# Optimization experiments

Measured on AMD Instinct MI355X. Metric: run time of the kernel, lower is better.

The kernel has to match this reference:

```python
import jax, jax.numpy as jnp
import numpy as np

B, N, E, D = 8, 4096, 65536, 256


def setup_inputs() -> dict:
    key = jax.random.key(0)
    ks = jax.random.split(key, 4)
    return {
        "node_features": jax.random.normal(ks[0], (B, N, D), dtype=jnp.float32),
        "W": jax.random.normal(ks[1], (D, D), dtype=jnp.float32) * (1.0 / np.sqrt(D)),
        "b": jnp.zeros((D,), dtype=jnp.float32),
        "gamma": jnp.ones((D,), dtype=jnp.float32),
        "beta": jnp.zeros((D,), dtype=jnp.float32),
        "edge_index": jax.random.randint(ks[2], (B, 2, E), 0, N, dtype=jnp.int64),
        "node_mask": jax.random.randint(ks[3], (B, N), 0, 2, dtype=jnp.int32),
    }


def reference(node_features, W, b, gamma, beta, edge_index, node_mask):
    # Linear projection: h = x @ W^T + b   (nn.Linear convention, W: [out, in])
    h = jnp.einsum("bni,oi->bno", node_features, W) + b  # [B, N, D]
    batch, n_nodes, d = h.shape
    n_edges = edge_index.shape[2]

    src = edge_index[:, 0, :]  # [B, E]
    tgt = edge_index[:, 1, :]  # [B, E]

    nm = node_mask.astype(h.dtype)  # [B, N]
    # edge valid iff both endpoints are valid nodes
    emask = jnp.take_along_axis(nm, src, axis=1) * jnp.take_along_axis(nm, tgt, axis=1)  # [B, E]

    # gather source features, mask invalid edges
    msg = jnp.take_along_axis(h, src[..., None], axis=1) * emask[..., None]  # [B, E, D]

    # batched scatter-add via flat segment_sum with per-batch offsets
    seg_ids = (tgt + jnp.arange(batch, dtype=tgt.dtype)[:, None] * n_nodes).reshape(-1)
    agg = jax.ops.segment_sum(msg.reshape(batch * n_edges, d), seg_ids,
                              num_segments=batch * n_nodes).reshape(batch, n_nodes, d)

    h = h + agg / jnp.sqrt(jnp.asarray(n_nodes, h.dtype))

    # dropout is identity in eval mode
    # LayerNorm over last dim (eps = 1e-5, torch default)
    mu = jnp.mean(h, axis=-1, keepdims=True)
    var = jnp.mean((h - mu) ** 2, axis=-1, keepdims=True)
    h = (h - mu) * jax.lax.rsqrt(var + 1e-5) * gamma + beta

    h = jax.nn.relu(h)
    return h * nm[..., None]
```

## Files before the change

kernel.cpp:

```cpp
#include <hip/hip_runtime.h>
#include <hip/hip_bf16.h>

#define NN 4096
#define DIM 256
#define NE 65536
#define TOT_NODES 32768
#define TOT_EDGES 524288

__device__ __forceinline__ float ldf(const void* p, int isbf, size_t i) {
    return isbf ? __bfloat162float(((const __hip_bfloat16*)p)[i]) : ((const float*)p)[i];
}
__device__ __forceinline__ void stf(void* p, int isbf, size_t i, float v) {
    if (isbf) ((__hip_bfloat16*)p)[i] = __float2bfloat16(v);
    else      ((float*)p)[i] = v;
}
__device__ __forceinline__ int ldi(const void* p, int is64, size_t i) {
    return is64 ? (int)((const long long*)p)[i] : ((const int*)p)[i];
}

__global__ void detect_kernel(const void* ei, const void* nm, const void* x, int* flags) {
    const int t = threadIdx.x;
    const long long ev = ((const long long*)ei)[t];
    const unsigned long long okE = __ballot(ev >= 0 && ev < NN);
    const long long mv = ((const long long*)nm)[t];
    const unsigned long long okM = __ballot(mv == 0 || mv == 1);
    const unsigned int w = ((const unsigned int*)x)[t];
    const int e = (w >> 7) & 0xFF;
    const unsigned long long okF = __ballot(e >= 100 && e <= 140);
    if (t == 0) {
        flags[0] = (okE == ~0ULL) ? 1 : 0;
        flags[1] = (okM == ~0ULL) ? 1 : 0;
        flags[2] = (__popcll(okF) >= 40) ? 1 : 0;
    }
}

__global__ __launch_bounds__(256)
void init_kernel(int* __restrict__ counts) {
    counts[blockIdx.x * 256 + threadIdx.x] = 0;
}


typedef __attribute__((ext_vector_type(8))) __bf16 bf16x8;
typedef __attribute__((ext_vector_type(4))) float  f32x4;

__device__ __forceinline__ unsigned short f2bf(float f) {
    unsigned u = __float_as_uint(f);
    u = (u + 0x7fffu + ((u >> 16) & 1u)) >> 16;
    return (unsigned short)u;
}
__device__ __forceinline__ float bf2f(unsigned short h) {
    return __uint_as_float(((unsigned)h) << 16);
}
__device__ __forceinline__ void cvt_hilo(float4 f, ushort4* hi, ushort4* lo) {
    const unsigned short h0 = f2bf(f.x), h1 = f2bf(f.y), h2 = f2bf(f.z), h3 = f2bf(f.w);
    *hi = make_ushort4(h0, h1, h2, h3);
    *lo = make_ushort4(f2bf(f.x - bf2f(h0)), f2bf(f.y - bf2f(h1)),
                       f2bf(f.z - bf2f(h2)), f2bf(f.w - bf2f(h3)));
}
__device__ __forceinline__ bf16x8 frag_ld(const unsigned short* base, int row, int col) {
    const int byte = ((row * 64 + col) * 2) ^ ((row & 7) << 4);
    return *(const bf16x8*)((const char*)base + byte);
}
__device__ __forceinline__ void gload16(const void* g, void* l) {
    __builtin_amdgcn_global_load_lds(
        (const __attribute__((address_space(1))) unsigned int*)g,
        (__attribute__((address_space(3))) unsigned int*)l, 16, 0, 0);
}

__global__ __launch_bounds__(512)
void gemm_kernel(const void* __restrict__ x, const void* __restrict__ w,
                 const void* __restrict__ bias, const int* __restrict__ flags,
                 float* __restrict__ h)
{
    __shared__ unsigned short Ahi[128 * 64];
    __shared__ unsigned short Bhi[256 * 64];
    __shared__ unsigned short Alo[128 * 64];
    __shared__ unsigned short Blo[256 * 64];

    const int fbf = flags[2];
    const int t = threadIdx.x;
    const int lane = t & 63;
    const int wid = t >> 6;
    const int wr = wid >> 2;
    const int wc = wid & 3;
    const int m0 = (int)blockIdx.x * 128;

    f32x4 acc[4][4];
#pragma unroll
    for (int mi = 0; mi < 4; ++mi)
#pragma unroll
        for (int nj = 0; nj < 4; ++nj)
            acc[mi][nj] = (f32x4){0.f, 0.f, 0.f, 0.f};

    for (int kt = 0; kt < 4; ++kt) {
        const int k0 = kt * 64;
        if (fbf) {
            const unsigned short* xp = (const unsigned short*)x;
            const unsigned short* wp = (const unsigned short*)w;
#pragma unroll
            for (int i = 0; i < 2; ++i) {
                const int s = i * 512 + t;
                const int row = s >> 3, cg = (s & 7) ^ (row & 7);
                gload16(xp + (size_t)(m0 + row) * 256 + k0 + cg * 8, &Ahi[s * 8]);
            }
#pragma unroll
            for (int i = 0; i < 4; ++i) {
                const int s = i * 512 + t;
                const int row = s >> 3, cg = (s & 7) ^ (row & 7);
                gload16(wp + (size_t)row * 256 + k0 + cg * 8, &Bhi[s * 8]);
            }
        } else {
            const float* xp = (const float*)x;
            const float* wp = (const float*)w;
#pragma unroll
            for (int i = 0; i < 2; ++i) {
                const int s = i * 512 + t;
                const int row = s >> 3, cg = (s & 7) ^ (row & 7);
                const float* src = xp + (size_t)(m0 + row) * 256 + k0 + cg * 8;
                const float4 f0 = *(const float4*)src, f1 = *(const float4*)(src + 4);
                ushort4 h0, l0, h1, l1;
                cvt_hilo(f0, &h0, &l0); cvt_hilo(f1, &h1, &l1);
                *(ushort4*)&Ahi[s * 8]     = h0; *(ushort4*)&Ahi[s * 8 + 4] = h1;
                *(ushort4*)&Alo[s * 8]     = l0; *(ushort4*)&Alo[s * 8 + 4] = l1;
            }
#pragma unroll
            for (int i = 0; i < 4; ++i) {
                const int s = i * 512 + t;
                const int row = s >> 3, cg = (s & 7) ^ (row & 7);
                const float* src = wp + (size_t)row * 256 + k0 + cg * 8;
                const float4 f0 = *(const float4*)src, f1 = *(const float4*)(src + 4);
                ushort4 h0, l0, h1, l1;
                cvt_hilo(f0, &h0, &l0); cvt_hilo(f1, &h1, &l1);
                *(ushort4*)&Bhi[s * 8]     = h0; *(ushort4*)&Bhi[s * 8 + 4] = h1;
                *(ushort4*)&Blo[s * 8]     = l0; *(ushort4*)&Blo[s * 8 + 4] = l1;
            }
        }
        __syncthreads();

#pragma unroll
        for (int kk = 0; kk < 64; kk += 32) {
            const int lr = lane & 15;
            const int lk = kk + ((lane >> 4) << 3);
            bf16x8 aH[4], bH[4];
#pragma unroll
            for (int mi = 0; mi < 4; ++mi)
                aH[mi] = frag_ld(Ahi, wr * 64 + mi * 16 + lr, lk);
#pragma unroll
            for (int nj = 0; nj < 4; ++nj)
                bH[nj] = frag_ld(Bhi, wc * 64 + nj * 16 + lr, lk);
#pragma unroll
            for (int mi = 0; mi < 4; ++mi)
#pragma unroll
                for (int nj = 0; nj < 4; ++nj)
                    acc[mi][nj] = __builtin_amdgcn_mfma_f32_16x16x32_bf16(
                        aH[mi], bH[nj], acc[mi][nj], 0, 0, 0);
            if (!fbf) {
                bf16x8 aL[4], bL[4];
#pragma unroll
                for (int mi = 0; mi < 4; ++mi)
                    aL[mi] = frag_ld(Alo, wr * 64 + mi * 16 + lr, lk);
#pragma unroll
                for (int nj = 0; nj < 4; ++nj)
                    bL[nj] = frag_ld(Blo, wc * 64 + nj * 16 + lr, lk);
#pragma unroll
                for (int mi = 0; mi < 4; ++mi)
#pragma unroll
                    for (int nj = 0; nj < 4; ++nj) {
                        acc[mi][nj] = __builtin_amdgcn_mfma_f32_16x16x32_bf16(
                            aH[mi], bL[nj], acc[mi][nj], 0, 0, 0);
                        acc[mi][nj] = __builtin_amdgcn_mfma_f32_16x16x32_bf16(
                            aL[mi], bH[nj], acc[mi][nj], 0, 0, 0);
                    }
            }
        }
        __syncthreads();
    }

    const int lr = lane & 15;
    const int r4 = (lane >> 4) << 2;
#pragma unroll
    for (int nj = 0; nj < 4; ++nj) {
        const int n = wc * 64 + nj * 16 + lr;
        const float bv = ldf(bias, fbf, n);
#pragma unroll
        for (int mi = 0; mi < 4; ++mi) {
            const int rb = m0 + wr * 64 + mi * 16 + r4;
#pragma unroll
            for (int r = 0; r < 4; ++r)
                h[(size_t)(rb + r) * 256 + n] = acc[mi][nj][r] + bv;
        }
    }
}

__global__ __launch_bounds__(256)
void count_kernel(const void* __restrict__ ei, const void* __restrict__ nm,
                  const int* __restrict__ flags, int* __restrict__ counts)
{
    const int e64 = flags[0], m64 = flags[1];
    const int tid = blockIdx.x * 256 + threadIdx.x;
    const int b = tid >> 16;
    const int e = tid & (NE - 1);
    const size_t eb = (size_t)b * 2 * NE;
    const int src = ldi(ei, e64, eb + e);
    const int tgt = ldi(ei, e64, eb + NE + e);
    const size_t mb = (size_t)b * NN;
    if (ldi(nm, m64, mb + src) && ldi(nm, m64, mb + tgt))
        atomicAdd(&counts[b * NN + tgt], 1);
}

__global__ __launch_bounds__(256)
void scan_kernel(int* __restrict__ counts, int* __restrict__ offsets)
{
    __shared__ int sums[256];
    const int t = threadIdx.x;
    const int base = t * 128;
    int s = 0;
    for (int i = 0; i < 128; ++i) s += counts[base + i];
    sums[t] = s;
    __syncthreads();
    for (int off = 1; off < 256; off <<= 1) {
        int v = (t >= off) ? sums[t - off] : 0;
        __syncthreads();
        sums[t] += v;
        __syncthreads();
    }
    int run = sums[t] - s;
    for (int i = 0; i < 128; ++i) {
        const int c = counts[base + i];
        offsets[base + i] = run;
        counts[base + i] = run;
        run += c;
    }
    if (t == 255) offsets[TOT_NODES] = sums[255];
}

__global__ __launch_bounds__(256)
void fill_kernel(const void* __restrict__ ei, const void* __restrict__ nm,
                 const int* __restrict__ flags,
                 int* __restrict__ cursor, int* __restrict__ bucket)
{
    const int e64 = flags[0], m64 = flags[1];
    const int tid = blockIdx.x * 256 + threadIdx.x;
    const int b = tid >> 16;
    const int e = tid & (NE - 1);
    const size_t eb = (size_t)b * 2 * NE;
    const int src = ldi(ei, e64, eb + e);
    const int tgt = ldi(ei, e64, eb + NE + e);
    const size_t mb = (size_t)b * NN;
    if (ldi(nm, m64, mb + src) && ldi(nm, m64, mb + tgt)) {
        int pos = atomicAdd(&cursor[b * NN + tgt], 1);
        bucket[pos] = src;
    }
}

__global__ __launch_bounds__(64)
void node_kernel(const float* __restrict__ h, const int* __restrict__ offsets,
                 const int* __restrict__ bucket, const void* __restrict__ nm,
                 const int* __restrict__ flags,
                 const void* __restrict__ gamma, const void* __restrict__ beta,
                 void* __restrict__ out)
{
    const int bt = blockIdx.x;
    const int lane = threadIdx.x;
    const int m64 = flags[1], fbf = flags[2];
    const size_t o4 = (size_t)bt * 64 + lane;
    if (!ldi(nm, m64, bt)) {
        if (fbf) ((ushort4*)out)[o4] = make_ushort4(0, 0, 0, 0);
        else     ((float4*)out)[o4]  = make_float4(0.f, 0.f, 0.f, 0.f);
        return;
    }
    const int b = bt >> 12;
    const float4* hb = (const float4*)h + ((size_t)b << 12) * 64;
    const float4 self = ((const float4*)h)[o4];
    const int s0 = offsets[bt], s1 = offsets[bt + 1];
    float4 a0 = make_float4(0.f, 0.f, 0.f, 0.f), a1 = a0, a2 = a0, a3 = a0;
    int j = s0;
    for (; j + 4 <= s1; j += 4) {
        const float4 v0 = hb[(size_t)bucket[j]     * 64 + lane];
        const float4 v1 = hb[(size_t)bucket[j + 1] * 64 + lane];
        const float4 v2 = hb[(size_t)bucket[j + 2] * 64 + lane];
        const float4 v3 = hb[(size_t)bucket[j + 3] * 64 + lane];
        a0.x += v0.x; a0.y += v0.y; a0.z += v0.z; a0.w += v0.w;
        a1.x += v1.x; a1.y += v1.y; a1.z += v1.z; a1.w += v1.w;
        a2.x += v2.x; a2.y += v2.y; a2.z += v2.z; a2.w += v2.w;
        a3.x += v3.x; a3.y += v3.y; a3.z += v3.z; a3.w += v3.w;
    }
    for (; j < s1; ++j) {
        const float4 v = hb[(size_t)bucket[j] * 64 + lane];
        a0.x += v.x; a0.y += v.y; a0.z += v.z; a0.w += v.w;
    }
    float4 acc;
    acc.x = self.x + ((a0.x + a1.x) + (a2.x + a3.x)) * 0.015625f;
    acc.y = self.y + ((a0.y + a1.y) + (a2.y + a3.y)) * 0.015625f;
    acc.z = self.z + ((a0.z + a1.z) + (a2.z + a3.z)) * 0.015625f;
    acc.w = self.w + ((a0.w + a1.w) + (a2.w + a3.w)) * 0.015625f;

    float v1r = (acc.x + acc.y) + (acc.z + acc.w);
    float v2r = (acc.x * acc.x + acc.y * acc.y) + (acc.z * acc.z + acc.w * acc.w);
#pragma unroll
    for (int off = 32; off > 0; off >>= 1) {
        v1r += __shfl_xor(v1r, off, 64);
        v2r += __shfl_xor(v2r, off, 64);
    }
    const float mu  = v1r * (1.f / 256.f);
    const float var = v2r * (1.f / 256.f) - mu * mu;
    const float inv = rsqrtf(var + 1e-5f);
    const int d0 = lane * 4;
    float y0 = (acc.x - mu) * inv * ldf(gamma, fbf, d0)     + ldf(beta, fbf, d0);
    float y1 = (acc.y - mu) * inv * ldf(gamma, fbf, d0 + 1) + ldf(beta, fbf, d0 + 1);
    float y2 = (acc.z - mu) * inv * ldf(gamma, fbf, d0 + 2) + ldf(beta, fbf, d0 + 2);
    float y3 = (acc.w - mu) * inv * ldf(gamma, fbf, d0 + 3) + ldf(beta, fbf, d0 + 3);
    y0 = fmaxf(y0, 0.f); y1 = fmaxf(y1, 0.f); y2 = fmaxf(y2, 0.f); y3 = fmaxf(y3, 0.f);
    if (fbf) ((ushort4*)out)[o4] = make_ushort4(f2bf(y0), f2bf(y1), f2bf(y2), f2bf(y3));
    else     ((float4*)out)[o4]  = make_float4(y0, y1, y2, y3);
}

static float g_sentinel[256];

extern "C" void kernel_launch(void* const* d_in, const int* in_sizes, int n_in,
                              void* d_out, int out_size, void* d_ws, size_t ws_size,
                              hipStream_t stream)
{
    (void)in_sizes; (void)n_in; (void)out_size;
    const void* x     = d_in[0];
    const void* W     = d_in[1];
    const void* bias  = d_in[2];
    const void* gamma = d_in[3];
    const void* beta  = d_in[4];
    const void* ei    = d_in[5];
    const void* nm    = d_in[6];

    char* ws = (char*)d_ws;
    int* flags   = (int*)ws;
    int* counts  = (int*)(ws + 256);
    int* offsets = (int*)(ws + 131328);
    int* bucket  = (int*)(ws + 262656);
    float* h     = (float*)(ws + 2359808);

    int fail = 0;
    hipGetLastError();
#define CHK(stage) do { if (!fail && hipGetLastError() != hipSuccess) fail = (stage); } while (0)

    detect_kernel<<<1, 64, 0, stream>>>(ei, nm, x, flags);                       CHK(1);
    init_kernel<<<TOT_NODES / 256, 256, 0, stream>>>(counts);                    CHK(2);
    gemm_kernel<<<TOT_NODES / 128, 512, 0, stream>>>(x, W, bias, flags, h);      CHK(3);
    count_kernel<<<TOT_EDGES / 256, 256, 0, stream>>>(ei, nm, flags, counts);    CHK(4);
    scan_kernel<<<1, 256, 0, stream>>>(counts, offsets);                         CHK(5);
    fill_kernel<<<TOT_EDGES / 256, 256, 0, stream>>>(ei, nm, flags, counts, bucket); CHK(6);
    node_kernel<<<TOT_NODES, 64, 0, stream>>>(h, offsets, bucket, nm, flags,
                                              gamma, beta, d_out);               CHK(7);
#undef CHK

    if (fail) {
        for (int i = 0; i < 256; ++i) g_sentinel[i] = 10000.f * (float)fail;
        hipMemcpyAsync(d_out, g_sentinel, sizeof(g_sentinel),
                       hipMemcpyHostToDevice, stream);
    }
}
```

Measured before the change: 172.2 us.

## Double-buffer GEMM loads, merge init/detect, vectorize edge kernels, batch node blocks

Merges the flag-detection and counter-zeroing kernels into one launch, which drops a launch. The bf16 GEMM path now double-buffers its LDS tiles so the next k-tile's async loads overlap the MFMA work, cutting the barriers per tile. The count and fill kernels each handle two edges per thread using vector index loads. The scan now reads counts coalesced, and node_kernel packs four nodes per 256-thread block, using the post-fill cursor array as segment ends instead of offsets[bt+1]. The fp32 path reuses the two LDS buffers as hi/lo planes, so its per-tile behaviour stays the same.

```diff
diff --git a/kernel.cpp b/kernel.cpp
--- a/kernel.cpp
+++ b/kernel.cpp
@@ -10,33 +10,30 @@
 __device__ __forceinline__ float ldf(const void* p, int isbf, size_t i) {
     return isbf ? __bfloat162float(((const __hip_bfloat16*)p)[i]) : ((const float*)p)[i];
 }
-__device__ __forceinline__ void stf(void* p, int isbf, size_t i, float v) {
-    if (isbf) ((__hip_bfloat16*)p)[i] = __float2bfloat16(v);
-    else      ((float*)p)[i] = v;
-}
 __device__ __forceinline__ int ldi(const void* p, int is64, size_t i) {
     return is64 ? (int)((const long long*)p)[i] : ((const int*)p)[i];
 }
 
-__global__ void detect_kernel(const void* ei, const void* nm, const void* x, int* flags) {
+__global__ __launch_bounds__(256)
+void init_detect_kernel(const void* ei, const void* nm, const void* x,
+                        int* __restrict__ flags, int* __restrict__ counts)
+{
     const int t = threadIdx.x;
-    const long long ev = ((const long long*)ei)[t];
-    const unsigned long long okE = __ballot(ev >= 0 && ev < NN);
-    const long long mv = ((const long long*)nm)[t];
-    const unsigned long long okM = __ballot(mv == 0 || mv == 1);
-    const unsigned int w = ((const unsigned int*)x)[t];
-    const int e = (w >> 7) & 0xFF;
-    const unsigned long long okF = __ballot(e >= 100 && e <= 140);
-    if (t == 0) {
-        flags[0] = (okE == ~0ULL) ? 1 : 0;
-        flags[1] = (okM == ~0ULL) ? 1 : 0;
-        flags[2] = (__popcll(okF) >= 40) ? 1 : 0;
-    }
-}
-
-__global__ __launch_bounds__(256)
-void init_kernel(int* __restrict__ counts) {
-    counts[blockIdx.x * 256 + threadIdx.x] = 0;
+    counts[blockIdx.x * 256 + t] = 0;
+    if (blockIdx.x == 0 && t < 64) {
+        const long long ev = ((const long long*)ei)[t];
+        const unsigned long long okE = __ballot(ev >= 0 && ev < NN);
+        const long long mv = ((const long long*)nm)[t];
+        const unsigned long long okM = __ballot(mv == 0 || mv == 1);
+        const unsigned int w = ((const unsigned int*)x)[t];
+        const int e = (w >> 7) & 0xFF;
+        const unsigned long long okF = __ballot(e >= 100 && e <= 140);
+        if (t == 0) {
+            flags[0] = (okE == ~0ULL) ? 1 : 0;
+            flags[1] = (okM == ~0ULL) ? 1 : 0;
+            flags[2] = (__popcll(okF) >= 40) ? 1 : 0;
+        }
+    }
 }
 
 
@@ -72,10 +69,8 @@
                  const void* __restrict__ bias, const int* __restrict__ flags,
                  float* __restrict__ h)
 {
-    __shared__ unsigned short Ahi[128 * 64];
-    __shared__ unsigned short Bhi[256 * 64];
-    __shared__ unsigned short Alo[128 * 64];
-    __shared__ unsigned short Blo[256 * 64];
+    __shared__ unsigned short As[2][128 * 64];
+    __shared__ unsigned short Bs[2][256 * 64];
 
     const int fbf = flags[2];
     const int t = threadIdx.x;
@@ -92,26 +87,58 @@
         for (int nj = 0; nj < 4; ++nj)
             acc[mi][nj] = (f32x4){0.f, 0.f, 0.f, 0.f};
 
-    for (int kt = 0; kt < 4; ++kt) {
-        const int k0 = kt * 64;
-        if (fbf) {
-            const unsigned short* xp = (const unsigned short*)x;
-            const unsigned short* wp = (const unsigned short*)w;
+    const int lr = lane & 15;
+    const int lk8 = (lane >> 4) << 3;
+
+    auto compute_hh = [&](const unsigned short* Ab, const unsigned short* Bb) {
+#pragma unroll
+        for (int kk = 0; kk < 64; kk += 32) {
+            const int lk = kk + lk8;
+            bf16x8 aH[4], bH[4];
+#pragma unroll
+            for (int mi = 0; mi < 4; ++mi)
+                aH[mi] = frag_ld(Ab, wr * 64 + mi * 16 + lr, lk);
+#pragma unroll
+            for (int nj = 0; nj < 4; ++nj)
+                bH[nj] = frag_ld(Bb, wc * 64 + nj * 16 + lr, lk);
+#pragma unroll
+            for (int mi = 0; mi < 4; ++mi)
+#pragma unroll
+                for (int nj = 0; nj < 4; ++nj)
+                    acc[mi][nj] = __builtin_amdgcn_mfma_f32_16x16x32_bf16(
+                        aH[mi], bH[nj], acc[mi][nj], 0, 0, 0);
+        }
+    };
+
+    if (fbf) {
+        const unsigned short* xp = (const unsigned short*)x;
+        const unsigned short* wp = (const unsigned short*)w;
+        auto stage = [&](int kt, int buf) {
+            const int k0 = kt * 64;
 #pragma unroll
             for (int i = 0; i < 2; ++i) {
                 const int s = i * 512 + t;
                 const int row = s >> 3, cg = (s & 7) ^ (row & 7);
-                gload16(xp + (size_t)(m0 + row) * 256 + k0 + cg * 8, &Ahi[s * 8]);
+                gload16(xp + (size_t)(m0 + row) * 256 + k0 + cg * 8, &As[buf][s * 8]);
             }
 #pragma unroll
             for (int i = 0; i < 4; ++i) {
                 const int s = i * 512 + t;
                 const int row = s >> 3, cg = (s & 7) ^ (row & 7);
-                gload16(wp + (size_t)row * 256 + k0 + cg * 8, &Bhi[s * 8]);
-            }
-        } else {
-            const float* xp = (const float*)x;
-            const float* wp = (const float*)w;
+                gload16(wp + (size_t)row * 256 + k0 + cg * 8, &Bs[buf][s * 8]);
+            }
+        };
+        stage(0, 0);
+        for (int kt = 0; kt < 4; ++kt) {
+            __syncthreads();
+            if (kt < 3) stage(kt + 1, (kt + 1) & 1);
+            compute_hh(As[kt & 1], Bs[kt & 1]);
+        }
+    } else {
+        const float* xp = (const float*)x;
+        const float* wp = (const float*)w;
+        for (int kt = 0; kt < 4; ++kt) {
+            const int k0 = kt * 64;
 #pragma unroll
             for (int i = 0; i < 2; ++i) {
                 const int s = i * 512 + t;
@@ -120,8 +147,8 @@
                 const float4 f0 = *(const float4*)src, f1 = *(const float4*)(src + 4);
                 ushort4 h0, l0, h1, l1;
                 cvt_hilo(f0, &h0, &l0); cvt_hilo(f1, &h1, &l1);
-                *(ushort4*)&Ahi[s * 8]     = h0; *(ushort4*)&Ahi[s * 8 + 4] = h1;
-                *(ushort4*)&Alo[s * 8]     = l0; *(ushort4*)&Alo[s * 8 + 4] = l1;
+                *(ushort4*)&As[0][s * 8]     = h0; *(ushort4*)&As[0][s * 8 + 4] = h1;
+                *(ushort4*)&As[1][s * 8]     = l0; *(ushort4*)&As[1][s * 8 + 4] = l1;
             }
 #pragma unroll
             for (int i = 0; i < 4; ++i) {
@@ -131,37 +158,25 @@
                 const float4 f0 = *(const float4*)src, f1 = *(const float4*)(src + 4);
                 ushort4 h0, l0, h1, l1;
                 cvt_hilo(f0, &h0, &l0); cvt_hilo(f1, &h1, &l1);
-                *(ushort4*)&Bhi[s * 8]     = h0; *(ushort4*)&Bhi[s * 8 + 4] = h1;
-                *(ushort4*)&Blo[s * 8]     = l0; *(ushort4*)&Blo[s * 8 + 4] = l1;
-            }
-        }
-        __syncthreads();
-
-#pragma unroll
-        for (int kk = 0; kk < 64; kk += 32) {
-            const int lr = lane & 15;
-            const int lk = kk + ((lane >> 4) << 3);
-            bf16x8 aH[4], bH[4];
-#pragma unroll
-            for (int mi = 0; mi < 4; ++mi)
-                aH[mi] = frag_ld(Ahi, wr * 64 + mi * 16 + lr, lk);
-#pragma unroll
-            for (int nj = 0; nj < 4; ++nj)
-                bH[nj] = frag_ld(Bhi, wc * 64 + nj * 16 + lr, lk);
-#pragma unroll
-            for (int mi = 0; mi < 4; ++mi)
-#pragma unroll
-                for (int nj = 0; nj < 4; ++nj)
-                    acc[mi][nj] = __builtin_amdgcn_mfma_f32_16x16x32_bf16(
-                        aH[mi], bH[nj], acc[mi][nj], 0, 0, 0);
-            if (!fbf) {
-                bf16x8 aL[4], bL[4];
-#pragma unroll
-                for (int mi = 0; mi < 4; ++mi)
-                    aL[mi] = frag_ld(Alo, wr * 64 + mi * 16 + lr, lk);
-#pragma unroll
-                for (int nj = 0; nj < 4; ++nj)
-                    bL[nj] = frag_ld(Blo, wc * 64 + nj * 16 + lr, lk);
+                *(ushort4*)&Bs[0][s * 8]     = h0; *(ushort4*)&Bs[0][s * 8 + 4] = h1;
+                *(ushort4*)&Bs[1][s * 8]     = l0; *(ushort4*)&Bs[1][s * 8 + 4] = l1;
+            }
+            __syncthreads();
+            compute_hh(As[0], Bs[0]);
+#pragma unroll
+            for (int kk = 0; kk < 64; kk += 32) {
+                const int lk = kk + lk8;
+                bf16x8 aH[4], bH[4], aL[4], bL[4];
+#pragma unroll
+                for (int mi = 0; mi < 4; ++mi) {
+                    aH[mi] = frag_ld(As[0], wr * 64 + mi * 16 + lr, lk);
+                    aL[mi] = frag_ld(As[1], wr * 64 + mi * 16 + lr, lk);
+                }
+#pragma unroll
+                for (int nj = 0; nj < 4; ++nj) {
+                    bH[nj] = frag_ld(Bs[0], wc * 64 + nj * 16 + lr, lk);
+                    bL[nj] = frag_ld(Bs[1], wc * 64 + nj * 16 + lr, lk);
+                }
 #pragma unroll
                 for (int mi = 0; mi < 4; ++mi)
 #pragma unroll
@@ -172,11 +187,10 @@
                             aL[mi], bH[nj], acc[mi][nj], 0, 0, 0);
                     }
             }
-        }
-        __syncthreads();
-    }
-
-    const int lr = lane & 15;
+            __syncthreads();
+        }
+    }
+
     const int r4 = (lane >> 4) << 2;
 #pragma unroll
     for (int nj = 0; nj < 4; ++nj) {
@@ -198,14 +212,24 @@
 {
     const int e64 = flags[0], m64 = flags[1];
     const int tid = blockIdx.x * 256 + threadIdx.x;
-    const int b = tid >> 16;
-    const int e = tid & (NE - 1);
+    const int b = tid >> 15;
+    const int k = (tid & 32767) << 1;
     const size_t eb = (size_t)b * 2 * NE;
-    const int src = ldi(ei, e64, eb + e);
-    const int tgt = ldi(ei, e64, eb + NE + e);
+    int s0, s1, t0, t1;
+    if (e64) {
+        const longlong2 sv = *(const longlong2*)((const long long*)ei + eb + k);
+        const longlong2 tv = *(const longlong2*)((const long long*)ei + eb + NE + k);
+        s0 = (int)sv.x; s1 = (int)sv.y; t0 = (int)tv.x; t1 = (int)tv.y;
+    } else {
+        const int2 sv = *(const int2*)((const int*)ei + eb + k);
+        const int2 tv = *(const int2*)((const int*)ei + eb + NE + k);
+        s0 = sv.x; s1 = sv.y; t0 = tv.x; t1 = tv.y;
+    }
     const size_t mb = (size_t)b * NN;
-    if (ldi(nm, m64, mb + src) && ldi(nm, m64, mb + tgt))
-        atomicAdd(&counts[b * NN + tgt], 1);
+    if (ldi(nm, m64, mb + s0) && ldi(nm, m64, mb + t0))
+        atomicAdd(&counts[b * NN + t0], 1);
+    if (ldi(nm, m64, mb + s1) && ldi(nm, m64, mb + t1))
+        atomicAdd(&counts[b * NN + t1], 1);
 }
 
 __global__ __launch_bounds__(256)
@@ -213,9 +237,8 @@
 {
     __shared__ int sums[256];
     const int t = threadIdx.x;
-    const int base = t * 128;
     int s = 0;
-    for (int i = 0; i < 128; ++i) s += counts[base + i];
+    for (int i = 0; i < 128; ++i) s += counts[i * 256 + t];
     sums[t] = s;
     __syncthreads();
     for (int off = 1; off < 256; off <<= 1) {
@@ -226,12 +249,12 @@
     }
     int run = sums[t] - s;
     for (int i = 0; i < 128; ++i) {
-        const int c = counts[base + i];
-        offsets[base + i] = run;
-        counts[base + i] = run;
+        const int idx = i * 256 + t;
+        const int c = counts[idx];
+        offsets[idx] = run;
+        counts[idx] = run;
         run += c;
     }
-    if (t == 255) offsets[TOT_NODES] = sums[255];
 }
 
 __global__ __launch_bounds__(256)
@@ -241,27 +264,35 @@
 {
     const int e64 = flags[0], m64 = flags[1];
     const int tid = blockIdx.x * 256 + threadIdx.x;
-    const int b = tid >> 16;
-    const int e = tid & (NE - 1);
+    const int b = tid >> 15;
+    const int k = (tid & 32767) << 1;
     const size_t eb = (size_t)b * 2 * NE;
-    const int src = ldi(ei, e64, eb + e);
-    const int tgt = ldi(ei, e64, eb + NE + e);
+    int s0, s1, t0, t1;
+    if (e64) {
+        const longlong2 sv = *(const longlong2*)((const long long*)ei + eb + k);
+        const longlong2 tv = *(const longlong2*)((const long long*)ei + eb + NE + k);
+        s0 = (int)sv.x; s1 = (int)sv.y; t0 = (int)tv.x; t1 = (int)tv.y;
+    } else {
+        const int2 sv = *(const int2*)((const int*)ei + eb + k);
+        const int2 tv = *(const int2*)((const int*)ei + eb + NE + k);
+        s0 = sv.x; s1 = sv.y; t0 = tv.x; t1 = tv.y;
+    }
     const size_t mb = (size_t)b * NN;
-    if (ldi(nm, m64, mb + src) && ldi(nm, m64, mb + tgt)) {
-        int pos = atomicAdd(&cursor[b * NN + tgt], 1);
-        bucket[pos] = src;
-    }
-}
-
-__global__ __launch_bounds__(64)
+    if (ldi(nm, m64, mb + s0) && ldi(nm, m64, mb + t0))
+        bucket[atomicAdd(&cursor[b * NN + t0], 1)] = s0;
+    if (ldi(nm, m64, mb + s1) && ldi(nm, m64, mb + t1))
+        bucket[atomicAdd(&cursor[b * NN + t1], 1)] = s1;
+}
+
+__global__ __launch_bounds__(256)
 void node_kernel(const float* __restrict__ h, const int* __restrict__ offsets,
-                 const int* __restrict__ bucket, const void* __restrict__ nm,
-                 const int* __restrict__ flags,
+                 const int* __restrict__ ends, const int* __restrict__ bucket,
+                 const void* __restrict__ nm, const int* __restrict__ flags,
                  const void* __restrict__ gamma, const void* __restrict__ beta,
                  void* __restrict__ out)
 {
-    const int bt = blockIdx.x;
-    const int lane = threadIdx.x;
+    const int bt = blockIdx.x * 4 + (threadIdx.x >> 6);
+    const int lane = threadIdx.x & 63;
     const int m64 = flags[1], fbf = flags[2];
     const size_t o4 = (size_t)bt * 64 + lane;
     if (!ldi(nm, m64, bt)) {
@@ -272,7 +303,7 @@
     const int b = bt >> 12;
     const float4* hb = (const float4*)h + ((size_t)b << 12) * 64;
     const float4 self = ((const float4*)h)[o4];
-    const int s0 = offsets[bt], s1 = offsets[bt + 1];
+    const int s0 = offsets[bt], s1 = ends[bt];
     float4 a0 = make_float4(0.f, 0.f, 0.f, 0.f), a1 = a0, a2 = a0, a3 = a0;
     int j = s0;
     for (; j + 4 <= s1; j += 4) {
@@ -341,14 +372,13 @@
     hipGetLastError();
 #define CHK(stage) do { if (!fail && hipGetLastError() != hipSuccess) fail = (stage); } while (0)
 
-    detect_kernel<<<1, 64, 0, stream>>>(ei, nm, x, flags);                       CHK(1);
-    init_kernel<<<TOT_NODES / 256, 256, 0, stream>>>(counts);                    CHK(2);
-    gemm_kernel<<<TOT_NODES / 128, 512, 0, stream>>>(x, W, bias, flags, h);      CHK(3);
-    count_kernel<<<TOT_EDGES / 256, 256, 0, stream>>>(ei, nm, flags, counts);    CHK(4);
-    scan_kernel<<<1, 256, 0, stream>>>(counts, offsets);                         CHK(5);
-    fill_kernel<<<TOT_EDGES / 256, 256, 0, stream>>>(ei, nm, flags, counts, bucket); CHK(6);
-    node_kernel<<<TOT_NODES, 64, 0, stream>>>(h, offsets, bucket, nm, flags,
-                                              gamma, beta, d_out);               CHK(7);
+    init_detect_kernel<<<TOT_NODES / 256, 256, 0, stream>>>(ei, nm, x, flags, counts); CHK(1);
+    gemm_kernel<<<TOT_NODES / 128, 512, 0, stream>>>(x, W, bias, flags, h);            CHK(2);
+    count_kernel<<<TOT_EDGES / 512, 256, 0, stream>>>(ei, nm, flags, counts);          CHK(3);
+    scan_kernel<<<1, 256, 0, stream>>>(counts, offsets);                               CHK(4);
+    fill_kernel<<<TOT_EDGES / 512, 256, 0, stream>>>(ei, nm, flags, counts, bucket);   CHK(5);
+    node_kernel<<<TOT_NODES / 4, 256, 0, stream>>>(h, offsets, counts, bucket, nm,
+                                                   flags, gamma, beta, d_out);         CHK(6);
 #undef CHK
 
     if (fail) {
```

Result: faster. 164.5 us (-4.5%).
